# Performance work log

Measured on AMD Instinct MI355X. Metric: run time of the kernel, lower is better.

Reference implementation:

```python
import jax, jax.numpy as jnp
import numpy as np

DIM = 256
HEADS = 8
DIM_HEAD = 64
INNER = HEADS * DIM_HEAD  # 512
SCALE = DIM_HEAD ** -0.5
B, H, W = 8, 64, 64


def setup_inputs() -> dict:
    key = jax.random.key(0)
    ks = jax.random.split(key, 6)
    x = jax.random.normal(ks[0], (B, DIM, H, W), dtype=jnp.float32)
    W_proj = jax.random.normal(ks[1], (DIM, INNER), dtype=jnp.float32) * (DIM ** -0.5)
    step_rep = jax.random.normal(ks[2], (HEADS, 1, 1), dtype=jnp.float32)
    step_x = jax.random.normal(ks[3], (HEADS, 1, 1), dtype=jnp.float32)
    W_out = jax.random.normal(ks[4], (INNER, DIM), dtype=jnp.float32) * (INNER ** -0.5)
    b_out = jax.random.normal(ks[5], (DIM,), dtype=jnp.float32) * 0.01
    return {"x": x, "W_proj": W_proj, "step_rep": step_rep, "step_x": step_x,
            "W_out": W_out, "b_out": b_out}


def _attention(q, k, v):
    # q: [b,h,m,d], k/v: [b,h,n,d]
    dots = jnp.einsum('bhmd,bhnd->bhmn', q, k) * SCALE
    attn = jax.nn.softmax(dots, axis=-1)
    out = jnp.einsum('bhmn,bhnd->bhmd', attn, v)
    return out, attn


def reference(x, W_proj, step_rep, step_x, W_out, b_out):
    b, c, h, w = x.shape
    n = h * w
    # b c h w -> b (h w) c
    x_seq = jnp.transpose(x, (0, 2, 3, 1)).reshape(b, n, c)
    proj = x_seq @ W_proj  # [b, n, inner]
    # AdaptiveAvgPool2d((8,8)) over the (h,w) grid; h,w divisible by 8 -> exact block mean
    proj_2d = proj.reshape(b, h, w, INNER)
    rep = proj_2d.reshape(b, 8, h // 8, 8, w // 8, INNER).mean(axis=(2, 4))  # [b,8,8,inner]
    rep = rep.reshape(b, 64, INNER)
    # split heads
    proj_h = proj.reshape(b, n, HEADS, DIM_HEAD).transpose(0, 2, 1, 3)  # [b,heads,n,dh]
    rep_h = rep.reshape(b, 64, HEADS, DIM_HEAD).transpose(0, 2, 1, 3)   # [b,heads,64,dh]
    # stage 1: 64 pooled queries attend to n keys
    rep_delta, attn = _attention(rep_h, proj_h, proj_h)  # attn: [b,heads,64,n]
    rep2 = rep_h + step_rep * rep_delta
    # stage 2: self-attention among the 64 pooled tokens
    x_delta, _ = _attention(rep2, rep2, rep2)  # [b,heads,64,dh]
    # back-project via attn^T
    x_delta = jnp.einsum('bhmn,bhmd->bhnd', attn, x_delta)  # [b,heads,n,dh]
    x_delta = step_x * x_delta
    # b h n k -> b n (h k)
    x_delta = x_delta.transpose(0, 2, 1, 3).reshape(b, n, INNER)
    x_out = x_delta @ W_out + b_out  # [b, n, dim]
    return x_out.reshape(b, h, w, c).transpose(0, 3, 1, 2)
```

## Files before the change

### kernel.cpp

```cpp
#include <hip/hip_runtime.h>
#include <cstdint>
#include <cstddef>


#define SCALE 0.125f

typedef __attribute__((ext_vector_type(8))) short bf16x8;
typedef __attribute__((ext_vector_type(4))) float f32x4;
typedef __attribute__((ext_vector_type(16))) float f32x16;
typedef __attribute__((ext_vector_type(4))) unsigned int u32x4;

#define MFMA32(a, b, c) __builtin_amdgcn_mfma_f32_32x32x16_bf16(a, b, c, 0, 0, 0)
#define MFMA16(a, b, c) __builtin_amdgcn_mfma_f32_16x16x32_bf16(a, b, c, 0, 0, 0)

__device__ __forceinline__ unsigned short f2bf(float x) {
  unsigned int u = __float_as_uint(x);
  u += 0x7FFFu + ((u >> 16) & 1u);
  return (unsigned short)(u >> 16);
}
__device__ __forceinline__ float bf2f(unsigned short b) {
  return __uint_as_float(((unsigned int)b) << 16);
}
__device__ __forceinline__ void split2(float x, unsigned short& h, unsigned short& l) {
  h = f2bf(x);
  l = f2bf(x - bf2f(h));
}
__device__ __forceinline__ unsigned int cvtpk(float lo, float hi_) {
  unsigned int r;
  asm("v_cvt_pk_bf16_f32 %0, %1, %2" : "=v"(r) : "v"(lo), "v"(hi_));
  return r;
}

typedef const __attribute__((address_space(1))) unsigned int* gas_ptr;
typedef __attribute__((address_space(3))) unsigned int* las_ptr;
__device__ __forceinline__ void gload16(const void* g, void* l) {
  __builtin_amdgcn_global_load_lds((gas_ptr)(size_t)g,
                                   (las_ptr)(unsigned int)(size_t)l, 16, 0, 0);
}

__global__ __launch_bounds__(256) void tsplit(
    const float* __restrict__ in, long long in_bs,
    unsigned short* __restrict__ oh, unsigned short* __restrict__ ol,
    long long o_bs, int R, int C) {
  __shared__ float T[32][33];
  int bz = blockIdx.z;
  const float* ip = in + (size_t)bz * in_bs;
  unsigned short* oph = oh + (size_t)bz * o_bs;
  unsigned short* opl = ol + (size_t)bz * o_bs;
  int c0 = blockIdx.x * 32, r0 = blockIdx.y * 32;
  int t = threadIdx.x;
  int col = t & 31, row8 = t >> 5;
#pragma unroll
  for (int i = 0; i < 4; i++)
    T[row8 + i * 8][col] = ip[(size_t)(r0 + row8 + i * 8) * C + c0 + col];
  __syncthreads();
#pragma unroll
  for (int i = 0; i < 4; i++) {
    float v = T[col][row8 + i * 8];
    unsigned short h, l;
    split2(v, h, l);
    size_t o = (size_t)(c0 + row8 + i * 8) * R + r0 + col;
    oph[o] = h;
    opl[o] = l;
  }
}

__global__ __launch_bounds__(256) void gemm_mfma(
    const unsigned short* __restrict__ Ah, const unsigned short* __restrict__ Al,
    long long a_bs,
    const unsigned short* __restrict__ Bh, const unsigned short* __restrict__ Bl,
    long long b_bs,
    float* __restrict__ Cf, unsigned short* __restrict__ Ch,
    unsigned short* __restrict__ Cl, long long c_bs,
    int M, int N, int K, const float* __restrict__ bias) {
  __shared__ unsigned short lds[4][128][32];
  int bz = blockIdx.z;
  int m0 = blockIdx.y * 128, n0 = blockIdx.x * 128;
  int t = threadIdx.x;
  int wave = t >> 6, lane = t & 63;
  int wr = wave >> 1, wc = wave & 1;

  const unsigned short* src;
  int r0g;
  if (wave == 0)      { src = Ah + (size_t)bz * a_bs; r0g = m0; }
  else if (wave == 1) { src = Al + (size_t)bz * a_bs; r0g = m0; }
  else if (wave == 2) { src = Bh + (size_t)bz * b_bs; r0g = n0; }
  else                { src = Bl + (size_t)bz * b_bs; r0g = n0; }
  int q = lane >> 2;
  int chunk = (lane & 3) ^ ((q >> 1) & 3);
  const unsigned short* srow = src + (size_t)(r0g + q) * K + chunk * 8;

  int g = lane >> 4, fr = lane & 15;
  int slot = (g ^ ((fr >> 1) & 3)) * 8;
  const unsigned short* aRow = &lds[0][wr * 64 + fr][slot];
  const unsigned short* bRow = &lds[2][wc * 64 + fr][slot];

  f32x4 acc[4][4];
#pragma unroll
  for (int i = 0; i < 4; i++)
#pragma unroll
    for (int j = 0; j < 4; j++)
#pragma unroll
      for (int r = 0; r < 4; r++) acc[i][j][r] = 0.0f;

  for (int k0 = 0; k0 < K; k0 += 32) {
    __syncthreads();
#pragma unroll
    for (int s = 0; s < 8; s++)
      gload16(srow + (size_t)(s * 16) * K + k0, &lds[wave][s * 16][0]);
    __syncthreads();
    bf16x8 af[2][4], bfv[2][4];
#pragma unroll
    for (int i = 0; i < 4; i++) {
      af[0][i]  = *(const bf16x8*)(aRow + i * 512);
      af[1][i]  = *(const bf16x8*)(aRow + 4096 + i * 512);
      bfv[0][i] = *(const bf16x8*)(bRow + i * 512);
      bfv[1][i] = *(const bf16x8*)(bRow + 4096 + i * 512);
    }
#pragma unroll
    for (int i = 0; i < 4; i++)
#pragma unroll
      for (int j = 0; j < 4; j++) {
        acc[i][j] = MFMA16(af[0][i], bfv[0][j], acc[i][j]);
        acc[i][j] = MFMA16(af[0][i], bfv[1][j], acc[i][j]);
        acc[i][j] = MFMA16(af[1][i], bfv[0][j], acc[i][j]);
      }
  }
  int mBase = m0 + wr * 64 + g * 4;
  int nBase = n0 + wc * 64 + fr;
  if (Cf) {
    float* Cb = Cf + (size_t)bz * c_bs;
#pragma unroll
    for (int i = 0; i < 4; i++)
#pragma unroll
      for (int qd = 0; qd < 4; qd++) {
        int m = mBase + i * 16 + qd;
        float bi = bias ? bias[m] : 0.0f;
#pragma unroll
        for (int j = 0; j < 4; j++)
          Cb[(size_t)m * N + nBase + j * 16] = acc[i][j][qd] + bi;
      }
  } else {
    unsigned short* Chb = Ch + (size_t)bz * c_bs;
    unsigned short* Clb = Cl + (size_t)bz * c_bs;
#pragma unroll
    for (int i = 0; i < 4; i++)
#pragma unroll
      for (int qd = 0; qd < 4; qd++) {
        int m = mBase + i * 16 + qd;
#pragma unroll
        for (int j = 0; j < 4; j++) {
          unsigned short hh, ll;
          split2(acc[i][j][qd], hh, ll);
          Chb[(size_t)m * N + nBase + j * 16] = hh;
          Clb[(size_t)m * N + nBase + j * 16] = ll;
        }
      }
  }
}

__global__ __launch_bounds__(256) void pool2_k(
    const unsigned short* __restrict__ projh, const unsigned short* __restrict__ projl,
    unsigned short* __restrict__ reph, unsigned short* __restrict__ repl) {
  int bp = blockIdx.x;
  int b = bp >> 6, p = bp & 63;
  int py = p >> 3, px = p & 7;
  int i0 = threadIdx.x * 2;
  float s0 = 0.0f, s1 = 0.0f;
  for (int dy = 0; dy < 8; dy++) {
    int hh = py * 8 + dy;
#pragma unroll
    for (int dx = 0; dx < 8; dx++) {
      int n = hh * 64 + px * 8 + dx;
      size_t o = ((size_t)(b * 4096 + n)) * 512 + i0;
      unsigned int wh = *(const unsigned int*)(projh + o);
      unsigned int wl = *(const unsigned int*)(projl + o);
      s0 += bf2f((unsigned short)wh) + bf2f((unsigned short)wl);
      s1 += bf2f((unsigned short)(wh >> 16)) + bf2f((unsigned short)(wl >> 16));
    }
  }
  s0 *= 0.015625f;
  s1 *= 0.015625f;
  unsigned short h0, l0, h1, l1;
  split2(s0, h0, l0);
  split2(s1, h1, l1);
  size_t ro = ((size_t)(b * 64 + p)) * 512 + i0;
  *(unsigned int*)(reph + ro) = (unsigned int)h0 | ((unsigned int)h1 << 16);
  *(unsigned int*)(repl + ro) = (unsigned int)l0 | ((unsigned int)l1 << 16);
}

__global__ __launch_bounds__(256) void fattn(
    const unsigned short* __restrict__ projh, const unsigned short* __restrict__ projl,
    const unsigned short* __restrict__ reph, const unsigned short* __restrict__ repl,
    unsigned short* __restrict__ PTh, unsigned short* __restrict__ PTl,
    float* __restrict__ pvpart, float* __restrict__ lpart) {
  int bh = blockIdx.x, s = blockIdx.y;
  int b = bh >> 3, h = bh & 7;
  int t = threadIdx.x;
  int wave = t >> 6, lane = t & 63;
  int lm = lane & 31, hi = lane >> 5;

  bf16x8 qf[2][4][2];
#pragma unroll
  for (int mt = 0; mt < 2; mt++)
#pragma unroll
    for (int ks = 0; ks < 4; ks++) {
      size_t qo = ((size_t)(b * 64 + mt * 32 + lm)) * 512 + h * 64 + ks * 16 + hi * 8;
      qf[mt][ks][0] = *(const bf16x8*)(reph + qo);
      qf[mt][ks][1] = *(const bf16x8*)(repl + qo);
    }

  f32x16 pv[2][2];
#pragma unroll
  for (int a = 0; a < 2; a++)
#pragma unroll
    for (int c = 0; c < 2; c++)
#pragma unroll
      for (int r = 0; r < 16; r++) pv[a][c][r] = 0.0f;
  float lsum0 = 0.0f, lsum1 = 0.0f;

  for (int sti = 0; sti < 2; sti++) {
    int n0 = s * 512 + (wave * 2 + sti) * 64;
    for (int nn = 0; nn < 64; nn += 32) {
      int nb = n0 + nn;
      f32x16 sa0, sa1;
#pragma unroll
      for (int r = 0; r < 16; r++) { sa0[r] = 0.0f; sa1[r] = 0.0f; }
#pragma unroll
      for (int ks = 0; ks < 4; ks++) {
        size_t ko = ((size_t)(b * 4096 + nb + lm)) * 512 + h * 64 + ks * 16 + hi * 8;
        bf16x8 kh = *(const bf16x8*)(projh + ko);
        bf16x8 kl = *(const bf16x8*)(projl + ko);
        sa0 = MFMA32(kh, qf[0][ks][0], sa0);
        sa0 = MFMA32(kh, qf[0][ks][1], sa0);
        sa0 = MFMA32(kl, qf[0][ks][0], sa0);
        sa1 = MFMA32(kh, qf[1][ks][0], sa1);
        sa1 = MFMA32(kh, qf[1][ks][1], sa1);
        sa1 = MFMA32(kl, qf[1][ks][0], sa1);
      }
#pragma unroll
      for (int r = 0; r < 16; r++) {
        sa0[r] = __expf(sa0[r] * SCALE); lsum0 += sa0[r];
        sa1[r] = __expf(sa1[r] * SCALE); lsum1 += sa1[r];
      }
      {
        int kk0 = h * 64 + lm, kk1 = kk0 + 32;
#pragma unroll
        for (int r = 0; r < 16; r++) {
          int n = nb + (r & 3) + 8 * (r >> 2) + 4 * hi;
          size_t o = ((size_t)(b * 4096 + n)) * 512;
          float p0 = sa0[r], p1 = sa1[r];
          unsigned short h0 = f2bf(p0), h1 = f2bf(p1);
          PTh[o + kk0] = h0; PTl[o + kk0] = f2bf(p0 - bf2f(h0));
          PTh[o + kk1] = h1; PTl[o + kk1] = f2bf(p1 - bf2f(h1));
        }
      }
#pragma unroll
      for (int kc = 0; kc < 2; kc++) {
        bf16x8 paH[2], paL[2];
#pragma unroll
        for (int mt = 0; mt < 2; mt++) {
          float pq[8], lq[8];
#pragma unroll
          for (int qi = 0; qi < 8; qi++) {
            float v = (mt == 0) ? sa0[kc * 8 + qi] : sa1[kc * 8 + qi];
            unsigned short ph_ = f2bf(v);
            pq[qi] = v;
            lq[qi] = v - bf2f(ph_);
          }
          int c01 = (int)cvtpk(pq[0], pq[1]), c23 = (int)cvtpk(pq[2], pq[3]);
          int c45 = (int)cvtpk(pq[4], pq[5]), c67 = (int)cvtpk(pq[6], pq[7]);
          int d01 = __shfl_xor(c01, 32), d23 = __shfl_xor(c23, 32);
          int d45 = __shfl_xor(c45, 32), d67 = __shfl_xor(c67, 32);
          u32x4 wv;
          wv.x = (unsigned int)(hi ? d45 : c01);
          wv.y = (unsigned int)(hi ? d67 : c23);
          wv.z = (unsigned int)(hi ? c45 : d01);
          wv.w = (unsigned int)(hi ? c67 : d23);
          paH[mt] = __builtin_bit_cast(bf16x8, wv);
          int e01 = (int)cvtpk(lq[0], lq[1]), e23 = (int)cvtpk(lq[2], lq[3]);
          int e45 = (int)cvtpk(lq[4], lq[5]), e67 = (int)cvtpk(lq[6], lq[7]);
          int f01 = __shfl_xor(e01, 32), f23 = __shfl_xor(e23, 32);
          int f45 = __shfl_xor(e45, 32), f67 = __shfl_xor(e67, 32);
          u32x4 lv;
          lv.x = (unsigned int)(hi ? f45 : e01);
          lv.y = (unsigned int)(hi ? f67 : e23);
          lv.z = (unsigned int)(hi ? e45 : f01);
          lv.w = (unsigned int)(hi ? e67 : f23);
          paL[mt] = __builtin_bit_cast(bf16x8, lv);
        }
#pragma unroll
        for (int dt = 0; dt < 2; dt++) {
          bf16x8 vh, vl;
#pragma unroll
          for (int j = 0; j < 8; j++) {
            size_t vo = ((size_t)(b * 4096 + nb + kc * 16 + hi * 8 + j)) * 512 +
                        h * 64 + dt * 32 + lm;
            vh[j] = (short)projh[vo];
            vl[j] = (short)projl[vo];
          }
          pv[0][dt] = MFMA32(paH[0], vh, pv[0][dt]);
          pv[0][dt] = MFMA32(paH[0], vl, pv[0][dt]);
          pv[0][dt] = MFMA32(paL[0], vh, pv[0][dt]);
          pv[1][dt] = MFMA32(paH[1], vh, pv[1][dt]);
          pv[1][dt] = MFMA32(paH[1], vl, pv[1][dt]);
          pv[1][dt] = MFMA32(paL[1], vh, pv[1][dt]);
        }
      }
    }
  }
  lsum0 += __shfl_xor(lsum0, 32);
  lsum1 += __shfl_xor(lsum1, 32);
  __shared__ float pvbuf[64][64];
  __shared__ float lbuf[4][64];
  if (hi == 0) { lbuf[wave][lm] = lsum0; lbuf[wave][32 + lm] = lsum1; }
  for (int w = 0; w < 4; w++) {
    __syncthreads();
    if (wave == w) {
#pragma unroll
      for (int mt = 0; mt < 2; mt++)
#pragma unroll
        for (int dt = 0; dt < 2; dt++)
#pragma unroll
          for (int r = 0; r < 16; r++) {
            int m = mt * 32 + (r & 3) + 8 * (r >> 2) + 4 * hi;
            int d = dt * 32 + lm;
            if (w == 0) pvbuf[m][d] = pv[mt][dt][r];
            else pvbuf[m][d] += pv[mt][dt][r];
          }
    }
  }
  __syncthreads();
  size_t base = ((size_t)(s * 64 + bh)) * 4096;
  for (int idx = t; idx < 4096; idx += 256)
    pvpart[base + idx] = pvbuf[idx >> 6][idx & 63];
  if (t < 64)
    lpart[((size_t)(s * 64 + bh)) * 64 + t] =
        lbuf[0][t] + lbuf[1][t] + lbuf[2][t] + lbuf[3][t];
}

__global__ __launch_bounds__(256) void merge_k(
    const float* __restrict__ pvpart, const float* __restrict__ lpart,
    const unsigned short* __restrict__ reph, const unsigned short* __restrict__ repl,
    const float* __restrict__ step_rep, float* __restrict__ rep2,
    float* __restrict__ linv) {
  int bh = blockIdx.x;
  int b = bh >> 3, h = bh & 7;
  float sr = step_rep[h];
  int t = threadIdx.x;
  __shared__ float lt[64];
  if (t < 64) {
    float L = 0.0f;
#pragma unroll
    for (int ss = 0; ss < 8; ss++) L += lpart[((size_t)(ss * 64 + bh)) * 64 + t];
    float inv = 1.0f / L;
    lt[t] = inv;
    linv[bh * 64 + t] = inv;
  }
  __syncthreads();
  for (int idx = t; idx < 4096; idx += 256) {
    int m = idx >> 6, d = idx & 63;
    float sum = 0.0f;
#pragma unroll
    for (int ss = 0; ss < 8; ss++)
      sum += pvpart[((size_t)(ss * 64 + bh)) * 4096 + idx];
    size_t ro = ((size_t)(b * 64 + m)) * 512 + h * 64 + d;
    float repv = bf2f(reph[ro]) + bf2f(repl[ro]);
    rep2[(size_t)bh * 4096 + idx] = repv + sr * sum * lt[m];
  }
}

__global__ __launch_bounds__(256) void stage2_k(
    const float* __restrict__ rep2, const float* __restrict__ Wo,
    const float* __restrict__ step_x, const float* __restrict__ linv,
    unsigned short* __restrict__ GTh, unsigned short* __restrict__ GTl) {
  __shared__ float T[64][68];
  __shared__ float P[64][68];
  __shared__ float Wl[64][68];
  int bh = blockIdx.x, h = bh & 7, b = bh >> 3;
  int t = threadIdx.x;
  int mi = t >> 2, dq = (t & 3) * 16;
#pragma unroll
  for (int j = 0; j < 4; j++) {
    float4 v = *(const float4*)(rep2 + ((size_t)bh * 64 + mi) * 64 + dq + j * 4);
    T[dq + j * 4 + 0][mi] = v.x; T[dq + j * 4 + 1][mi] = v.y;
    T[dq + j * 4 + 2][mi] = v.z; T[dq + j * 4 + 3][mi] = v.w;
  }
  __syncthreads();
  int tx = t & 15, ty = t >> 4;
  {
    float acc[4][4] = {};
#pragma unroll
    for (int k = 0; k < 64; k++) {
      float4 a = *(const float4*)&T[k][ty * 4];
      float4 bv = *(const float4*)&T[k][tx * 4];
      float aa[4] = {a.x, a.y, a.z, a.w};
      float bb[4] = {bv.x, bv.y, bv.z, bv.w};
#pragma unroll
      for (int i = 0; i < 4; i++)
#pragma unroll
        for (int j = 0; j < 4; j++) acc[i][j] += aa[i] * bb[j];
    }
#pragma unroll
    for (int i = 0; i < 4; i++)
      *(float4*)&P[ty * 4 + i][tx * 4] =
          make_float4(acc[i][0] * SCALE, acc[i][1] * SCALE, acc[i][2] * SCALE,
                      acc[i][3] * SCALE);
  }
  __syncthreads();
  if (t < 64) {
    float mx = -3.4e38f;
    for (int n = 0; n < 64; n++) mx = fmaxf(mx, P[t][n]);
    float s = 0.0f;
    for (int n = 0; n < 64; n++) {
      float e = __expf(P[t][n] - mx);
      P[t][n] = e;
      s += e;
    }
    float r = 1.0f / s;
    for (int n = 0; n < 64; n++) P[t][n] *= r;
  }
  __syncthreads();
  float xacc[4][4] = {};
#pragma unroll
  for (int k = 0; k < 64; k++) {
    float aa[4], bb[4];
#pragma unroll
    for (int i = 0; i < 4; i++) {
      aa[i] = P[ty * 4 + i][k];
      bb[i] = T[tx * 4 + i][k];
    }
#pragma unroll
    for (int i = 0; i < 4; i++)
#pragma unroll
      for (int j = 0; j < 4; j++) xacc[i][j] += aa[i] * bb[j];
  }
  __syncthreads();
#pragma unroll
  for (int i = 0; i < 4; i++)
    *(float4*)&P[ty * 4 + i][tx * 4] =
        make_float4(xacc[i][0], xacc[i][1], xacc[i][2], xacc[i][3]);
  float sxh = step_x[h];
  float li[4];
#pragma unroll
  for (int i = 0; i < 4; i++) li[i] = linv[bh * 64 + ty * 4 + i] * sxh;
  int wk = t >> 2, wcq = (t & 3) * 16;
  for (int cb = 0; cb < 4; cb++) {
    __syncthreads();
#pragma unroll
    for (int j = 0; j < 4; j++)
      *(float4*)&Wl[wk][wcq + j * 4] =
          *(const float4*)(Wo + ((size_t)(h * 64 + wk)) * 256 + cb * 64 + wcq + j * 4);
    __syncthreads();
    float gacc[4][4] = {};
#pragma unroll
    for (int k = 0; k < 64; k++) {
      float aa[4];
#pragma unroll
      for (int i = 0; i < 4; i++) aa[i] = P[ty * 4 + i][k];
      float4 bv = *(const float4*)&Wl[k][tx * 4];
      float bb[4] = {bv.x, bv.y, bv.z, bv.w};
#pragma unroll
      for (int i = 0; i < 4; i++)
#pragma unroll
        for (int j = 0; j < 4; j++) gacc[i][j] += aa[i] * bb[j];
    }
#pragma unroll
    for (int i = 0; i < 4; i++)
#pragma unroll
      for (int j = 0; j < 4; j++) {
        float val = gacc[i][j] * li[i];
        size_t o = ((size_t)(b * 256 + cb * 64 + tx * 4 + j)) * 512 + h * 64 + ty * 4 + i;
        unsigned short hh, ll;
        split2(val, hh, ll);
        GTh[o] = hh;
        GTl[o] = ll;
      }
  }
}

extern "C" void kernel_launch(void* const* d_in, const int* in_sizes, int n_in,
                              void* d_out, int out_size, void* d_ws, size_t ws_size,
                              hipStream_t stream) {
  const float* x = (const float*)d_in[0];
  const float* Wp = (const float*)d_in[1];
  const float* srep = (const float*)d_in[2];
  const float* sx = (const float*)d_in[3];
  const float* Wo = (const float*)d_in[4];
  const float* bo = (const float*)d_in[5];
  float* out = (float*)d_out;

  char* wsb = (char*)d_ws;
  unsigned short* projh = (unsigned short*)(wsb + 0);
  unsigned short* projl = (unsigned short*)(wsb + 33554432);
  unsigned short* xTh   = (unsigned short*)(wsb + 67108864);
  unsigned short* xTl   = (unsigned short*)(wsb + 83886080);
  unsigned short* PTh   = (unsigned short*)(wsb + 67108864);
  unsigned short* PTl   = (unsigned short*)(wsb + 100663296);
  unsigned short* WpTh  = (unsigned short*)(wsb + 100663296);
  unsigned short* WpTl  = (unsigned short*)(wsb + 100925440);
  unsigned short* reph  = (unsigned short*)(wsb + 134217728);
  unsigned short* repl  = (unsigned short*)(wsb + 134742016);
  float*  pvpart        = (float*)(wsb + 135266304);
  float*  lpart         = (float*)(wsb + 143654912);
  float*  rep2          = (float*)(wsb + 0);
  float*  linv          = (float*)(wsb + 1048576);
  unsigned short* GTh   = (unsigned short*)(wsb + 2097152);
  unsigned short* GTl   = (unsigned short*)(wsb + 4194304);

  tsplit<<<dim3(128, 8, 8), 256, 0, stream>>>(x, (long long)256 * 4096,
                                              xTh, xTl, (long long)4096 * 256, 256, 4096);
  tsplit<<<dim3(16, 8, 1), 256, 0, stream>>>(Wp, 0, WpTh, WpTl, 0, 256, 512);
  gemm_mfma<<<dim3(4, 32, 8), 256, 0, stream>>>(
      xTh, xTl, (long long)4096 * 256, WpTh, WpTl, 0,
      nullptr, projh, projl, (long long)4096 * 512, 4096, 512, 256, nullptr);
  pool2_k<<<dim3(512), 256, 0, stream>>>(projh, projl, reph, repl);
  fattn<<<dim3(64, 8), 256, 0, stream>>>(projh, projl, reph, repl, PTh, PTl,
                                         pvpart, lpart);
  merge_k<<<dim3(64), 256, 0, stream>>>(pvpart, lpart, reph, repl, srep, rep2, linv);
  stage2_k<<<dim3(64), 256, 0, stream>>>(rep2, Wo, sx, linv, GTh, GTl);
  gemm_mfma<<<dim3(32, 2, 8), 256, 0, stream>>>(
      GTh, GTl, (long long)256 * 512, PTh, PTl, (long long)4096 * 512,
      out, nullptr, nullptr, (long long)256 * 4096, 256, 4096, 512, bo);
}
```

Measured before the change: 253.6 us.

## Double-buffer GEMM, drop low-part terms, transpose proj for V, parallelize merge

New measurement: 236.7 us. 1.07x faster.

```diff
diff --git a/kernel.cpp b/kernel.cpp
--- a/kernel.cpp
+++ b/kernel.cpp
@@ -54,17 +54,21 @@
   for (int i = 0; i < 4; i++)
     T[row8 + i * 8][col] = ip[(size_t)(r0 + row8 + i * 8) * C + c0 + col];
   __syncthreads();
-#pragma unroll
-  for (int i = 0; i < 4; i++) {
-    float v = T[col][row8 + i * 8];
-    unsigned short h, l;
-    split2(v, h, l);
-    size_t o = (size_t)(c0 + row8 + i * 8) * R + r0 + col;
-    oph[o] = h;
-    opl[o] = l;
-  }
-}
-
+  int cp = (t & 15) * 2, rr = t >> 4;
+#pragma unroll
+  for (int i = 0; i < 2; i++) {
+    int orow = rr + i * 16;
+    float v0 = T[cp][orow], v1 = T[cp + 1][orow];
+    unsigned short h0, l0, h1, l1;
+    split2(v0, h0, l0);
+    split2(v1, h1, l1);
+    size_t o = (size_t)(c0 + orow) * R + r0 + cp;
+    *(unsigned int*)(oph + o) = (unsigned int)h0 | ((unsigned int)h1 << 16);
+    *(unsigned int*)(opl + o) = (unsigned int)l0 | ((unsigned int)l1 << 16);
+  }
+}
+
+template <int BT>
 __global__ __launch_bounds__(256) void gemm_mfma(
     const unsigned short* __restrict__ Ah, const unsigned short* __restrict__ Al,
     long long a_bs,
@@ -72,28 +76,39 @@
     long long b_bs,
     float* __restrict__ Cf, unsigned short* __restrict__ Ch,
     unsigned short* __restrict__ Cl, long long c_bs,
-    int M, int N, int K, const float* __restrict__ bias) {
-  __shared__ unsigned short lds[4][128][32];
-  int bz = blockIdx.z;
-  int m0 = blockIdx.y * 128, n0 = blockIdx.x * 128;
-  int t = threadIdx.x;
-  int wave = t >> 6, lane = t & 63;
+    int M, int N, int K, const float* __restrict__ bias, int lnx, int lny) {
+  __shared__ unsigned short lds[2][4][128][32];
+  int id0 = blockIdx.x;
+  int cpx = gridDim.x >> 3;
+  int id = (id0 & 7) * cpx + (id0 >> 3);
+  int bx = id & ((1 << lnx) - 1);
+  int by = (id >> lnx) & ((1 << lny) - 1);
+  int bz = id >> (lnx + lny);
+  int m0 = by * 128, n0 = bx * 128;
+  int tid = threadIdx.x;
+  int wave = tid >> 6, lane = tid & 63;
   int wr = wave >> 1, wc = wave & 1;
 
   const unsigned short* src;
-  int r0g;
-  if (wave == 0)      { src = Ah + (size_t)bz * a_bs; r0g = m0; }
-  else if (wave == 1) { src = Al + (size_t)bz * a_bs; r0g = m0; }
-  else if (wave == 2) { src = Bh + (size_t)bz * b_bs; r0g = n0; }
-  else                { src = Bl + (size_t)bz * b_bs; r0g = n0; }
+  int r0g, sBeg = 0, nS = 8, dArr = wave;
+  if (wave == 0) {
+    src = Ah + (size_t)bz * a_bs; r0g = m0;
+  } else if (wave == 1) {
+    src = Al + (size_t)bz * a_bs; r0g = m0;
+  } else if (BT == 2) {
+    src = ((wave == 2) ? Bh : Bl) + (size_t)bz * b_bs; r0g = n0;
+  } else {
+    src = Bh + (size_t)bz * b_bs; r0g = n0; dArr = 2;
+    sBeg = (wave - 2) * 4; nS = 4;
+  }
   int q = lane >> 2;
   int chunk = (lane & 3) ^ ((q >> 1) & 3);
   const unsigned short* srow = src + (size_t)(r0g + q) * K + chunk * 8;
 
   int g = lane >> 4, fr = lane & 15;
   int slot = (g ^ ((fr >> 1) & 3)) * 8;
-  const unsigned short* aRow = &lds[0][wr * 64 + fr][slot];
-  const unsigned short* bRow = &lds[2][wc * 64 + fr][slot];
+  int offA = (wr * 64 + fr) * 32 + slot;
+  int offB = 2 * 4096 + (wc * 64 + fr) * 32 + slot;
 
   f32x4 acc[4][4];
 #pragma unroll
@@ -103,28 +118,40 @@
 #pragma unroll
       for (int r = 0; r < 4; r++) acc[i][j][r] = 0.0f;
 
-  for (int k0 = 0; k0 < K; k0 += 32) {
-    __syncthreads();
-#pragma unroll
-    for (int s = 0; s < 8; s++)
-      gload16(srow + (size_t)(s * 16) * K + k0, &lds[wave][s * 16][0]);
-    __syncthreads();
+  int nt = K >> 5;
+  for (int s5 = 0; s5 < nS; ++s5) {
+    int ss = sBeg + s5;
+    gload16(srow + (size_t)(ss * 16) * K, &lds[0][dArr][ss * 16][0]);
+  }
+  __syncthreads();
+  int cur = 0;
+  for (int t0 = 0; t0 < nt; ++t0) {
+    if (t0 + 1 < nt) {
+      int k0 = (t0 + 1) << 5;
+      for (int s5 = 0; s5 < nS; ++s5) {
+        int ss = sBeg + s5;
+        gload16(srow + (size_t)(ss * 16) * K + k0, &lds[cur ^ 1][dArr][ss * 16][0]);
+      }
+    }
+    const unsigned short* bb = &lds[cur][0][0][0];
     bf16x8 af[2][4], bfv[2][4];
 #pragma unroll
     for (int i = 0; i < 4; i++) {
-      af[0][i]  = *(const bf16x8*)(aRow + i * 512);
-      af[1][i]  = *(const bf16x8*)(aRow + 4096 + i * 512);
-      bfv[0][i] = *(const bf16x8*)(bRow + i * 512);
-      bfv[1][i] = *(const bf16x8*)(bRow + 4096 + i * 512);
+      af[0][i] = *(const bf16x8*)(bb + offA + i * 512);
+      af[1][i] = *(const bf16x8*)(bb + 4096 + offA + i * 512);
+      bfv[0][i] = *(const bf16x8*)(bb + offB + i * 512);
+      if (BT == 2) bfv[1][i] = *(const bf16x8*)(bb + 4096 + offB + i * 512);
     }
 #pragma unroll
     for (int i = 0; i < 4; i++)
 #pragma unroll
       for (int j = 0; j < 4; j++) {
         acc[i][j] = MFMA16(af[0][i], bfv[0][j], acc[i][j]);
-        acc[i][j] = MFMA16(af[0][i], bfv[1][j], acc[i][j]);
+        if (BT == 2) acc[i][j] = MFMA16(af[0][i], bfv[1][j], acc[i][j]);
         acc[i][j] = MFMA16(af[1][i], bfv[0][j], acc[i][j]);
       }
+    __syncthreads();
+    cur ^= 1;
   }
   int mBase = m0 + wr * 64 + g * 4;
   int nBase = n0 + wc * 64 + fr;
@@ -159,40 +186,70 @@
   }
 }
 
-__global__ __launch_bounds__(256) void pool2_k(
+__global__ __launch_bounds__(256) void tpool(
     const unsigned short* __restrict__ projh, const unsigned short* __restrict__ projl,
+    unsigned short* __restrict__ projTh,
     unsigned short* __restrict__ reph, unsigned short* __restrict__ repl) {
-  int bp = blockIdx.x;
-  int b = bp >> 6, p = bp & 63;
-  int py = p >> 3, px = p & 7;
-  int i0 = threadIdx.x * 2;
-  float s0 = 0.0f, s1 = 0.0f;
+  __shared__ unsigned short Lh[64][64];
+  __shared__ unsigned short Ll[64][64];
+  int it = blockIdx.x, py = blockIdx.y, b = blockIdx.z;
+  int t = threadIdx.x;
+  int ch = t & 63, seg = t >> 6;
+  int swc = ((ch ^ (ch >> 3)) & 7) << 3;
+  float poolacc[2] = {0.0f, 0.0f};
+
   for (int dy = 0; dy < 8; dy++) {
-    int hh = py * 8 + dy;
-#pragma unroll
-    for (int dx = 0; dx < 8; dx++) {
-      int n = hh * 64 + px * 8 + dx;
-      size_t o = ((size_t)(b * 4096 + n)) * 512 + i0;
-      unsigned int wh = *(const unsigned int*)(projh + o);
-      unsigned int wl = *(const unsigned int*)(projl + o);
-      s0 += bf2f((unsigned short)wh) + bf2f((unsigned short)wl);
-      s1 += bf2f((unsigned short)(wh >> 16)) + bf2f((unsigned short)(wl >> 16));
-    }
-  }
-  s0 *= 0.015625f;
-  s1 *= 0.015625f;
-  unsigned short h0, l0, h1, l1;
-  split2(s0, h0, l0);
-  split2(s1, h1, l1);
-  size_t ro = ((size_t)(b * 64 + p)) * 512 + i0;
-  *(unsigned int*)(reph + ro) = (unsigned int)h0 | ((unsigned int)h1 << 16);
-  *(unsigned int*)(repl + ro) = (unsigned int)l0 | ((unsigned int)l1 << 16);
+    int base_n = py * 512 + dy * 64;
+    {
+      int rl = t >> 3, cq = (t & 7) * 8;
+#pragma unroll
+      for (int p = 0; p < 2; p++) {
+        int row = rl + p * 32;
+        size_t ga = ((size_t)(b * 4096 + base_n + row)) * 512 + it * 64 + cq;
+        bf16x8 vh = *(const bf16x8*)(projh + ga);
+        bf16x8 vl = *(const bf16x8*)(projl + ga);
+#pragma unroll
+        for (int j = 0; j < 8; j++) {
+          int cl = cq + j;
+          int sw = ((cl ^ (cl >> 3)) & 7) << 3;
+          Lh[cl][row ^ sw] = (unsigned short)vh[j];
+          Ll[cl][row ^ sw] = (unsigned short)vl[j];
+        }
+      }
+    }
+    __syncthreads();
+#pragma unroll
+    for (int half = 0; half < 2; half++) {
+      int n0 = seg * 16 + half * 8;
+      int n0x = n0 ^ swc;
+      bf16x8 rh = *(const bf16x8*)&Lh[ch][n0x];
+      bf16x8 rl8 = *(const bf16x8*)&Ll[ch][n0x];
+      size_t o = ((size_t)(b * 512 + it * 64 + ch)) * 4096 + base_n + n0;
+      *(bf16x8*)(projTh + o) = rh;
+      float ssum = 0.0f;
+#pragma unroll
+      for (int j = 0; j < 8; j++)
+        ssum += bf2f((unsigned short)rh[j]) + bf2f((unsigned short)rl8[j]);
+      poolacc[half] += ssum;
+    }
+    __syncthreads();
+  }
+#pragma unroll
+  for (int half = 0; half < 2; half++) {
+    float v = poolacc[half] * 0.015625f;
+    unsigned short hh, ll;
+    split2(v, hh, ll);
+    size_t ro = ((size_t)(b * 64 + py * 8 + seg * 2 + half)) * 512 + it * 64 + ch;
+    reph[ro] = hh;
+    repl[ro] = ll;
+  }
 }
 
 __global__ __launch_bounds__(256) void fattn(
-    const unsigned short* __restrict__ projh, const unsigned short* __restrict__ projl,
+    const unsigned short* __restrict__ projh,
     const unsigned short* __restrict__ reph, const unsigned short* __restrict__ repl,
-    unsigned short* __restrict__ PTh, unsigned short* __restrict__ PTl,
+    const unsigned short* __restrict__ projTh,
+    unsigned short* __restrict__ PTh,
     float* __restrict__ pvpart, float* __restrict__ lpart) {
   int bh = blockIdx.x, s = blockIdx.y;
   int b = bh >> 3, h = bh & 7;
@@ -221,23 +278,23 @@
 
   for (int sti = 0; sti < 2; sti++) {
     int n0 = s * 512 + (wave * 2 + sti) * 64;
+#pragma unroll
     for (int nn = 0; nn < 64; nn += 32) {
       int nb = n0 + nn;
       f32x16 sa0, sa1;
 #pragma unroll
       for (int r = 0; r < 16; r++) { sa0[r] = 0.0f; sa1[r] = 0.0f; }
+      __builtin_amdgcn_s_setprio(1);
 #pragma unroll
       for (int ks = 0; ks < 4; ks++) {
         size_t ko = ((size_t)(b * 4096 + nb + lm)) * 512 + h * 64 + ks * 16 + hi * 8;
         bf16x8 kh = *(const bf16x8*)(projh + ko);
-        bf16x8 kl = *(const bf16x8*)(projl + ko);
         sa0 = MFMA32(kh, qf[0][ks][0], sa0);
         sa0 = MFMA32(kh, qf[0][ks][1], sa0);
-        sa0 = MFMA32(kl, qf[0][ks][0], sa0);
         sa1 = MFMA32(kh, qf[1][ks][0], sa1);
         sa1 = MFMA32(kh, qf[1][ks][1], sa1);
-        sa1 = MFMA32(kl, qf[1][ks][0], sa1);
-      }
+      }
+      __builtin_amdgcn_s_setprio(0);
 #pragma unroll
       for (int r = 0; r < 16; r++) {
         sa0[r] = __expf(sa0[r] * SCALE); lsum0 += sa0[r];
@@ -249,10 +306,8 @@
         for (int r = 0; r < 16; r++) {
           int n = nb + (r & 3) + 8 * (r >> 2) + 4 * hi;
           size_t o = ((size_t)(b * 4096 + n)) * 512;
-          float p0 = sa0[r], p1 = sa1[r];
-          unsigned short h0 = f2bf(p0), h1 = f2bf(p1);
-          PTh[o + kk0] = h0; PTl[o + kk0] = f2bf(p0 - bf2f(h0));
-          PTh[o + kk1] = h1; PTl[o + kk1] = f2bf(p1 - bf2f(h1));
+          PTh[o + kk0] = f2bf(sa0[r]);
+          PTh[o + kk1] = f2bf(sa1[r]);
         }
       }
 #pragma unroll
@@ -291,20 +346,15 @@
         }
 #pragma unroll
         for (int dt = 0; dt < 2; dt++) {
-          bf16x8 vh, vl;
-#pragma unroll
-          for (int j = 0; j < 8; j++) {
-            size_t vo = ((size_t)(b * 4096 + nb + kc * 16 + hi * 8 + j)) * 512 +
-                        h * 64 + dt * 32 + lm;
-            vh[j] = (short)projh[vo];
-            vl[j] = (short)projl[vo];
-          }
+          size_t vto = ((size_t)(b * 512 + h * 64 + dt * 32 + lm)) * 4096 +
+                       nb + kc * 16 + hi * 8;
+          bf16x8 vh = *(const bf16x8*)(projTh + vto);
+          __builtin_amdgcn_s_setprio(1);
           pv[0][dt] = MFMA32(paH[0], vh, pv[0][dt]);
-          pv[0][dt] = MFMA32(paH[0], vl, pv[0][dt]);
           pv[0][dt] = MFMA32(paL[0], vh, pv[0][dt]);
           pv[1][dt] = MFMA32(paH[1], vh, pv[1][dt]);
-          pv[1][dt] = MFMA32(paH[1], vl, pv[1][dt]);
           pv[1][dt] = MFMA32(paL[1], vh, pv[1][dt]);
+          __builtin_amdgcn_s_setprio(0);
         }
       }
     }
@@ -344,7 +394,7 @@
     const unsigned short* __restrict__ reph, const unsigned short* __restrict__ repl,
     const float* __restrict__ step_rep, float* __restrict__ rep2,
     float* __restrict__ linv) {
-  int bh = blockIdx.x;
+  int bh = blockIdx.x, qy = blockIdx.y;
   int b = bh >> 3, h = bh & 7;
   float sr = step_rep[h];
   int t = threadIdx.x;
@@ -355,10 +405,12 @@
     for (int ss = 0; ss < 8; ss++) L += lpart[((size_t)(ss * 64 + bh)) * 64 + t];
     float inv = 1.0f / L;
     lt[t] = inv;
-    linv[bh * 64 + t] = inv;
-  }
-  __syncthreads();
-  for (int idx = t; idx < 4096; idx += 256) {
+    if (qy == 0) linv[bh * 64 + t] = inv;
+  }
+  __syncthreads();
+#pragma unroll
+  for (int k2 = 0; k2 < 4; k2++) {
+    int idx = qy * 1024 + k2 * 256 + t;
     int m = idx >> 6, d = idx & 63;
     float sum = 0.0f;
 #pragma unroll
@@ -495,10 +547,10 @@
   unsigned short* projl = (unsigned short*)(wsb + 33554432);
   unsigned short* xTh   = (unsigned short*)(wsb + 67108864);
   unsigned short* xTl   = (unsigned short*)(wsb + 83886080);
-  unsigned short* PTh   = (unsigned short*)(wsb + 67108864);
-  unsigned short* PTl   = (unsigned short*)(wsb + 100663296);
+  unsigned short* projTh= (unsigned short*)(wsb + 67108864);
   unsigned short* WpTh  = (unsigned short*)(wsb + 100663296);
   unsigned short* WpTl  = (unsigned short*)(wsb + 100925440);
+  unsigned short* PTh   = (unsigned short*)(wsb + 100663296);
   unsigned short* reph  = (unsigned short*)(wsb + 134217728);
   unsigned short* repl  = (unsigned short*)(wsb + 134742016);
   float*  pvpart        = (float*)(wsb + 135266304);
@@ -511,15 +563,18 @@
   tsplit<<<dim3(128, 8, 8), 256, 0, stream>>>(x, (long long)256 * 4096,
                                               xTh, xTl, (long long)4096 * 256, 256, 4096);
   tsplit<<<dim3(16, 8, 1), 256, 0, stream>>>(Wp, 0, WpTh, WpTl, 0, 256, 512);
-  gemm_mfma<<<dim3(4, 32, 8), 256, 0, stream>>>(
+  gemm_mfma<2><<<dim3(1024), 256, 0, stream>>>(
       xTh, xTl, (long long)4096 * 256, WpTh, WpTl, 0,
-      nullptr, projh, projl, (long long)4096 * 512, 4096, 512, 256, nullptr);
-  pool2_k<<<dim3(512), 256, 0, stream>>>(projh, projl, reph, repl);
-  fattn<<<dim3(64, 8), 256, 0, stream>>>(projh, projl, reph, repl, PTh, PTl,
+      nullptr, projh, projl, (long long)4096 * 512, 4096, 512, 256, nullptr,
+      2, 5);
+  tpool<<<dim3(8, 8, 8), 256, 0, stream>>>(projh, projl, projTh, reph, repl);
+  fattn<<<dim3(64, 8), 256, 0, stream>>>(projh, reph, repl, projTh, PTh,
                                          pvpart, lpart);
-  merge_k<<<dim3(64), 256, 0, stream>>>(pvpart, lpart, reph, repl, srep, rep2, linv);
+  merge_k<<<dim3(64, 4), 256, 0, stream>>>(pvpart, lpart, reph, repl, srep,
+                                           rep2, linv);
   stage2_k<<<dim3(64), 256, 0, stream>>>(rep2, Wo, sx, linv, GTh, GTl);
-  gemm_mfma<<<dim3(32, 2, 8), 256, 0, stream>>>(
-      GTh, GTl, (long long)256 * 512, PTh, PTl, (long long)4096 * 512,
-      out, nullptr, nullptr, (long long)256 * 4096, 256, 4096, 512, bo);
-}
+  gemm_mfma<1><<<dim3(512), 256, 0, stream>>>(
+      GTh, GTl, (long long)256 * 512, PTh, nullptr, (long long)4096 * 512,
+      out, nullptr, nullptr, (long long)256 * 4096, 256, 4096, 512, bo,
+      5, 1);
+}
```
